# Performance work log

Hardware: AMD Instinct MI355X
Metric: run time of the kernel (lower is better)

## Reference

```python
import jax, jax.numpy as jnp
import numpy as np

B, N, C, H = 8, 4096, 384, 8
HD = C // H  # 48
KERNEL_EPS = 1e-3
EPS = 1e-8


def setup_inputs() -> dict:
    key = jax.random.key(0)
    k1, k2, k3, k4 = jax.random.split(key, 4)
    x = jax.random.normal(k1, (B, N, C), dtype=jnp.float32)
    Wqkv = jax.random.normal(k2, (3 * C, C), dtype=jnp.float32) * 0.02
    Wproj = jax.random.normal(k3, (C, C), dtype=jnp.float32) * 0.02
    bproj = jax.random.normal(k4, (C,), dtype=jnp.float32) * 0.02
    return {"x": x, "Wqkv": Wqkv, "Wproj": Wproj, "bproj": bproj}


def reference(x, Wqkv, Wproj, bproj):
    # qkv projection (no bias): (B,N,3C) -> (3,B,H,N,HD)
    qkv = jnp.einsum('bnc,dc->bnd', x, Wqkv).reshape(B, N, 3, H, HD)
    qkv = jnp.transpose(qkv, (2, 0, 3, 1, 4))
    q, k, v = qkv[0], qkv[1], qkv[2]

    # generalized_kernel with projection_matrix=None, kernel_fn=ReLU
    dn = HD ** (-0.25)  # data normalizer
    qp = jax.nn.relu(dn * q) + KERNEL_EPS  # (B,H,N,HD) feature map, m=HD
    kp = jax.nn.relu(dn * k) + KERNEL_EPS

    ks = kp.sum(axis=2)                              # (B,H,m)
    D = jnp.einsum('bhnm,bhm->bhn', qp, ks)          # (B,H,N)
    kptv = jnp.einsum('bhnd,bhnm->bhdm', v, kp)      # (B,H,HD,m)
    out = jnp.einsum('bhnm,bhdm->bhnd', qp, kptv) / (D[..., None] + EPS)

    # faithful to original: reshape (B,H,N,HD) -> (B,N,C) WITHOUT head transpose
    out = out.reshape(B, N, C)
    return jnp.einsum('bnc,dc->bnd', out, Wproj) + bproj
```

## Files before the change

kernel.cpp:

```cpp
#include <hip/hip_runtime.h>
#include <hip/hip_bf16.h>


typedef __attribute__((ext_vector_type(8))) short short8;
typedef __attribute__((ext_vector_type(4))) float floatx4;

#define MFMA(a, b, c) __builtin_amdgcn_mfma_f32_16x16x32_bf16((a), (b), (c), 0, 0, 0)

__device__ __forceinline__ unsigned short f2bf(float f) {
  union { float f; unsigned u; } x; x.f = f;
  unsigned r = x.u + 0x7FFFu + ((x.u >> 16) & 1u);
  return (unsigned short)(r >> 16);
}

__device__ __forceinline__ void cv4(const float* __restrict__ in, unsigned short* __restrict__ out, int i) {
  float4 v = *(const float4*)(in + i);
  uint2 o;
  o.x = (unsigned)f2bf(v.x) | ((unsigned)f2bf(v.y) << 16);
  o.y = (unsigned)f2bf(v.z) | ((unsigned)f2bf(v.w) << 16);
  *(uint2*)(out + i) = o;
}

__global__ void conv_w(const float* __restrict__ wq, const float* __restrict__ wp,
                       unsigned short* __restrict__ wqb, unsigned short* __restrict__ wpb,
                       float* __restrict__ accD) {
  const int tid = blockIdx.x * blockDim.x + threadIdx.x;
  const int stride = gridDim.x * blockDim.x * 4;
  for (int i = tid * 4; i < 442368; i += stride) cv4(wq, wqb, i);
  for (int i = tid * 4; i < 147456; i += stride) cv4(wp, wpb, i);
  float4 z = {0.f, 0.f, 0.f, 0.f};
  for (int i = tid * 4; i < 196608; i += stride) *(float4*)(accD + i) = z;
}

__global__ __launch_bounds__(256, 2) void gemm_qkv(
    const float* __restrict__ x,
    const unsigned short* __restrict__ Wq,
    unsigned short* __restrict__ qp,
    float* __restrict__ accD) {
  __shared__ unsigned short As[128 * 64];
  __shared__ unsigned short Bs[128 * 64];
  __shared__ unsigned short Tt[2][48 * 136];

  const int cpx = gridDim.x >> 3;
  const int bid = (blockIdx.x & 7) * cpx + (blockIdx.x >> 3);
  const int mt = bid / 11;
  const int j = bid - mt * 11;
  const int tid = threadIdx.x;
  const int w = tid >> 6, lane = tid & 63;
  const int wm = w >> 1, wn = w & 1;
  const int l15 = lane & 15, l4 = lane >> 4;
  const int isQ = (j < 3);
  const int h = j - 3;

  floatx4 zero = {0.f, 0.f, 0.f, 0.f};
  floatx4 acc[4][4];
#pragma unroll
  for (int i = 0; i < 4; ++i)
#pragma unroll
    for (int jj = 0; jj < 4; ++jj) acc[i][jj] = zero;

  const size_t Abase = (size_t)mt * 128 * 384;
  const int arow = tid >> 4;
  const int akf = (tid & 15) * 4;

  for (int k0 = 0; k0 < 384; k0 += 64) {
#pragma unroll
    for (int p = 0; p < 8; ++p) {
      int row = p * 16 + arow;
      float4 v = *(const float4*)&x[Abase + (size_t)row * 384 + k0 + akf];
      uint2 o;
      o.x = (unsigned)f2bf(v.x) | ((unsigned)f2bf(v.y) << 16);
      o.y = (unsigned)f2bf(v.z) | ((unsigned)f2bf(v.w) << 16);
      *(uint2*)&As[row * 64 + akf] = o;
    }
    if (isQ) {
      const size_t Bb = (size_t)(j * 128) * 384;
#pragma unroll
      for (int i = 0; i < 4; ++i) {
        int li = w * 256 + i * 64 + lane;
        int row = li >> 3, col = (li & 7) << 3;
        __builtin_amdgcn_global_load_lds(
            (const __attribute__((address_space(1))) void*)(Wq + Bb + (size_t)row * 384 + k0 + col),
            (__attribute__((address_space(3))) void*)&Bs[row * 64 + col], 16, 0, 0);
      }
    } else {
#pragma unroll
      for (int i = 0; i < 3; ++i) {
        int idx = i * 256 + tid;
        int row = idx >> 3, col = (idx & 7) << 3;
        int srow = (row < 48) ? (384 + h * 48 + row) : (720 + h * 48 + row);
        __builtin_amdgcn_global_load_lds(
            (const __attribute__((address_space(1))) void*)(Wq + (size_t)srow * 384 + k0 + col),
            (__attribute__((address_space(3))) void*)&Bs[row * 64 + col], 16, 0, 0);
      }
    }
    __syncthreads();
#pragma unroll
    for (int kk = 0; kk < 2; ++kk) {
      short8 a[4];
#pragma unroll
      for (int mf = 0; mf < 4; ++mf)
        a[mf] = *(const short8*)&As[(wm * 64 + mf * 16 + l15) * 64 + kk * 32 + l4 * 8];
      if (isQ) {
#pragma unroll
        for (int nf = 0; nf < 4; ++nf) {
          short8 b = *(const short8*)&Bs[(wn * 64 + nf * 16 + l15) * 64 + kk * 32 + l4 * 8];
#pragma unroll
          for (int mf = 0; mf < 4; ++mf) acc[mf][nf] = MFMA(a[mf], b, acc[mf][nf]);
        }
      } else {
#pragma unroll
        for (int nf = 0; nf < 3; ++nf) {
          short8 b = *(const short8*)&Bs[(wn * 48 + nf * 16 + l15) * 64 + kk * 32 + l4 * 8];
#pragma unroll
          for (int mf = 0; mf < 4; ++mf) acc[mf][nf] = MFMA(a[mf], b, acc[mf][nf]);
        }
      }
    }
    __syncthreads();
  }

  const float DN = 0.3799178430f;
  if (isQ) {
#pragma unroll
    for (int mf = 0; mf < 4; ++mf) {
#pragma unroll
      for (int nf = 0; nf < 4; ++nf) {
        int gm0 = mt * 128 + wm * 64 + mf * 16 + l4 * 4;
        int gn = j * 128 + wn * 64 + nf * 16 + l15;
#pragma unroll
        for (int r = 0; r < 4; ++r) {
          float v = fmaxf(acc[mf][nf][r] * DN, 0.f) + 1e-3f;
          qp[(size_t)(gm0 + r) * 384 + gn] = f2bf(v);
        }
      }
    }
  } else {
#pragma unroll
    for (int nf = 0; nf < 3; ++nf) {
#pragma unroll
      for (int mf = 0; mf < 4; ++mf) {
#pragma unroll
        for (int r = 0; r < 4; ++r) {
          float v = acc[mf][nf][r];
          if (wn == 0) v = fmaxf(v * DN, 0.f) + 1e-3f;
          Tt[wn][(nf * 16 + l15) * 136 + wm * 64 + mf * 16 + l4 * 4 + r] = f2bf(v);
        }
      }
    }
    __syncthreads();
    short8 ones;
    {
      unsigned short ov = (l15 == 0) ? (unsigned short)0x3F80 : (unsigned short)0;
#pragma unroll
      for (int e = 0; e < 8; ++e) ones[e] = (short)ov;
    }
    floatx4 acc2[3];
#pragma unroll
    for (int i = 0; i < 3; ++i) acc2[i] = zero;
#pragma unroll
    for (int c = 0; c < 4; ++c) {
      short8 af;
      if (w < 3)
        af = *(const short8*)&Tt[1][(w * 16 + l15) * 136 + c * 32 + l4 * 8];
      else
        af = ones;
#pragma unroll
      for (int mfr = 0; mfr < 3; ++mfr) {
        short8 bf8 = *(const short8*)&Tt[0][(mfr * 16 + l15) * 136 + c * 32 + l4 * 8];
        acc2[mfr] = MFMA(af, bf8, acc2[mfr]);
      }
    }
    float* dst = accD + (size_t)((mt >> 5) * 8 + h) * 3072;
    if (w < 3) {
#pragma unroll
      for (int mfr = 0; mfr < 3; ++mfr)
#pragma unroll
        for (int r = 0; r < 4; ++r)
          atomicAdd(&dst[(w * 16 + l4 * 4 + r) * 48 + mfr * 16 + l15], acc2[mfr][r]);
    } else if (l4 == 0) {
#pragma unroll
      for (int mfr = 0; mfr < 3; ++mfr)
        atomicAdd(&dst[48 * 48 + mfr * 16 + l15], acc2[mfr][0]);
    }
  }
}

__global__ __launch_bounds__(256, 2) void attn_out(
    const unsigned short* __restrict__ qp,
    const float* __restrict__ accD,
    unsigned short* __restrict__ outr) {
  const int bh = blockIdx.x >> 4, tg = blockIdx.x & 15;
  const int b = bh >> 3, h = bh & 7;
  const int tid = threadIdx.x, w = tid >> 6, lane = tid & 63;
  const int l15 = lane & 15, l4 = lane >> 4;
  const int t0 = tg * 256 + w * 64;

  short8 bfr[2][4];
#pragma unroll
  for (int kk = 0; kk < 2; ++kk) {
#pragma unroll
    for (int nf = 0; nf < 4; ++nf) {
      int row = nf * 16 + l15;
      int c0 = kk * 32 + l4 * 8;
      short8 f;
      if (kk == 1 && l4 >= 2) {
#pragma unroll
        for (int e = 0; e < 8; ++e) f[e] = 0;
      } else {
        const float* p = accD + (size_t)bh * 3072 + row * 48 + c0;
        float4 v0 = *(const float4*)p;
        float4 v1 = *(const float4*)(p + 4);
        f[0] = (short)f2bf(v0.x); f[1] = (short)f2bf(v0.y);
        f[2] = (short)f2bf(v0.z); f[3] = (short)f2bf(v0.w);
        f[4] = (short)f2bf(v1.x); f[5] = (short)f2bf(v1.y);
        f[6] = (short)f2bf(v1.z); f[7] = (short)f2bf(v1.w);
      }
      bfr[kk][nf] = f;
    }
  }

  floatx4 zero = {0.f, 0.f, 0.f, 0.f};
  floatx4 acc[4][4];
#pragma unroll
  for (int i = 0; i < 4; ++i)
#pragma unroll
    for (int j = 0; j < 4; ++j) acc[i][j] = zero;

  const size_t rb = (size_t)b * 4096;
#pragma unroll
  for (int mf = 0; mf < 4; ++mf) {
#pragma unroll
    for (int kk = 0; kk < 2; ++kk) {
      int tt = t0 + mf * 16 + l15;
      short8 a = *(const short8*)&qp[(rb + tt) * 384 + h * 48 + kk * 32 + l4 * 8];
#pragma unroll
      for (int nf = 0; nf < 4; ++nf)
        acc[mf][nf] = MFMA(a, bfr[kk][nf], acc[mf][nf]);
    }
  }

#pragma unroll
  for (int mf = 0; mf < 4; ++mf) {
    float den[4];
#pragma unroll
    for (int r = 0; r < 4; ++r)
      den[r] = __shfl(acc[mf][3][r], lane & 48, 64) + 1e-8f;
#pragma unroll
    for (int nf = 0; nf < 3; ++nf) {
#pragma unroll
      for (int r = 0; r < 4; ++r) {
        int tt = t0 + mf * 16 + l4 * 4 + r;
        int d = nf * 16 + l15;
        float v = acc[mf][nf][r] / den[r];
        int np = h * 512 + (tt >> 3);
        int cp = (tt & 7) * 48 + d;
        outr[(rb + np) * 384 + cp] = f2bf(v);
      }
    }
  }
}

__global__ __launch_bounds__(256, 2) void gemm_proj(
    const unsigned short* __restrict__ A,
    const unsigned short* __restrict__ Bt,
    float* __restrict__ Cout,
    const float* __restrict__ bias) {
  __shared__ unsigned short As[128 * 64];
  __shared__ unsigned short Bs[128 * 64];
  const int NT = 3;
  const int cpx = gridDim.x >> 3;
  const int bid = (blockIdx.x & 7) * cpx + (blockIdx.x >> 3);
  const int bn = bid % NT;
  const int bm = bid / NT;
  const int tid = threadIdx.x;
  const int w = tid >> 6, lane = tid & 63;
  const int wm = w >> 1, wn = w & 1;
  const int l15 = lane & 15, l4 = lane >> 4;

  floatx4 zero = {0.f, 0.f, 0.f, 0.f};
  floatx4 acc[4][4];
#pragma unroll
  for (int i = 0; i < 4; ++i)
#pragma unroll
    for (int j = 0; j < 4; ++j) acc[i][j] = zero;

  const int li0 = (w * 4) * 64 + lane;
  const size_t Abase = (size_t)(bm * 128) * 384;
  const size_t Bbase = (size_t)(bn * 128) * 384;

  for (int k0 = 0; k0 < 384; k0 += 64) {
#pragma unroll
    for (int i = 0; i < 4; ++i) {
      int li = li0 + i * 64;
      int row = li >> 3;
      int col = (li & 7) << 3;
      __builtin_amdgcn_global_load_lds(
          (const __attribute__((address_space(1))) void*)(A + Abase + (size_t)row * 384 + k0 + col),
          (__attribute__((address_space(3))) void*)&As[(w * 4 + i) * 512], 16, 0, 0);
      __builtin_amdgcn_global_load_lds(
          (const __attribute__((address_space(1))) void*)(Bt + Bbase + (size_t)row * 384 + k0 + col),
          (__attribute__((address_space(3))) void*)&Bs[(w * 4 + i) * 512], 16, 0, 0);
    }
    __syncthreads();
#pragma unroll
    for (int kk = 0; kk < 2; ++kk) {
      short8 a[4], b[4];
#pragma unroll
      for (int mf = 0; mf < 4; ++mf)
        a[mf] = *(const short8*)&As[(wm * 64 + mf * 16 + l15) * 64 + kk * 32 + l4 * 8];
#pragma unroll
      for (int nf = 0; nf < 4; ++nf)
        b[nf] = *(const short8*)&Bs[(wn * 64 + nf * 16 + l15) * 64 + kk * 32 + l4 * 8];
#pragma unroll
      for (int mf = 0; mf < 4; ++mf)
#pragma unroll
        for (int nf = 0; nf < 4; ++nf)
          acc[mf][nf] = MFMA(a[mf], b[nf], acc[mf][nf]);
    }
    __syncthreads();
  }

#pragma unroll
  for (int mf = 0; mf < 4; ++mf) {
#pragma unroll
    for (int nf = 0; nf < 4; ++nf) {
      int gm0 = bm * 128 + wm * 64 + mf * 16 + l4 * 4;
      int gn = bn * 128 + wn * 64 + nf * 16 + l15;
#pragma unroll
      for (int r = 0; r < 4; ++r)
        Cout[(size_t)(gm0 + r) * 384 + gn] = acc[mf][nf][r] + bias[gn];
    }
  }
}

extern "C" void kernel_launch(void* const* d_in, const int* in_sizes, int n_in,
                              void* d_out, int out_size, void* d_ws, size_t ws_size,
                              hipStream_t stream) {
  const float* x = (const float*)d_in[0];
  const float* Wqkv = (const float*)d_in[1];
  const float* Wproj = (const float*)d_in[2];
  const float* bproj = (const float*)d_in[3];

  char* ws = (char*)d_ws;
  unsigned short* qp = (unsigned short*)(ws);
  float* accD = (float*)(ws + 25165824);
  unsigned short* outr = (unsigned short*)(ws + 25952256);
  unsigned short* wqkvb = (unsigned short*)(ws + 51118080);
  unsigned short* wprojb = (unsigned short*)(ws + 52002816);

  conv_w<<<256, 256, 0, stream>>>(Wqkv, Wproj, wqkvb, wprojb, accD);
  gemm_qkv<<<2816, 256, 0, stream>>>(x, wqkvb, qp, accD);
  attn_out<<<1024, 256, 0, stream>>>(qp, accD, outr);
  gemm_proj<<<768, 256, 0, stream>>>(outr, wprojb, (float*)d_out, bproj);
}
```

Measured before the change: 207.4 us.

## Prefetch x tiles into registers, stage qp in LDS, use reciprocal for normalization

In the QKV GEMM, the next k-step's fp32 x tile is loaded into registers right after the barrier, so the global load overlaps the MFMA work. The bf16 conversion and LDS store of that tile move to the next iteration. The K/V feature-map stores to LDS are packed into 64-bit writes. In attn_out, each block's 256x48 qp tile is staged through padded shared memory instead of per-lane strided global loads, and the division by the denominator becomes a hardware reciprocal plus multiply, which slightly lowers precision and raises register use.

```diff
diff --git a/kernel.cpp b/kernel.cpp
--- a/kernel.cpp
+++ b/kernel.cpp
@@ -63,16 +63,12 @@
   const int arow = tid >> 4;
   const int akf = (tid & 15) * 4;
 
+  float4 xv[8];
+#pragma unroll
+  for (int p = 0; p < 8; ++p)
+    xv[p] = *(const float4*)&x[Abase + (size_t)(p * 16 + arow) * 384 + akf];
+
   for (int k0 = 0; k0 < 384; k0 += 64) {
-#pragma unroll
-    for (int p = 0; p < 8; ++p) {
-      int row = p * 16 + arow;
-      float4 v = *(const float4*)&x[Abase + (size_t)row * 384 + k0 + akf];
-      uint2 o;
-      o.x = (unsigned)f2bf(v.x) | ((unsigned)f2bf(v.y) << 16);
-      o.y = (unsigned)f2bf(v.z) | ((unsigned)f2bf(v.w) << 16);
-      *(uint2*)&As[row * 64 + akf] = o;
-    }
     if (isQ) {
       const size_t Bb = (size_t)(j * 128) * 384;
 #pragma unroll
@@ -94,7 +90,20 @@
             (__attribute__((address_space(3))) void*)&Bs[row * 64 + col], 16, 0, 0);
       }
     }
-    __syncthreads();
+#pragma unroll
+    for (int p = 0; p < 8; ++p) {
+      int row = p * 16 + arow;
+      uint2 o;
+      o.x = (unsigned)f2bf(xv[p].x) | ((unsigned)f2bf(xv[p].y) << 16);
+      o.y = (unsigned)f2bf(xv[p].z) | ((unsigned)f2bf(xv[p].w) << 16);
+      *(uint2*)&As[row * 64 + akf] = o;
+    }
+    __syncthreads();
+    if (k0 < 320) {
+#pragma unroll
+      for (int p = 0; p < 8; ++p)
+        xv[p] = *(const float4*)&x[Abase + (size_t)(p * 16 + arow) * 384 + k0 + 64 + akf];
+    }
 #pragma unroll
     for (int kk = 0; kk < 2; ++kk) {
       short8 a[4];
@@ -140,12 +149,18 @@
     for (int nf = 0; nf < 3; ++nf) {
 #pragma unroll
       for (int mf = 0; mf < 4; ++mf) {
-#pragma unroll
-        for (int r = 0; r < 4; ++r) {
-          float v = acc[mf][nf][r];
-          if (wn == 0) v = fmaxf(v * DN, 0.f) + 1e-3f;
-          Tt[wn][(nf * 16 + l15) * 136 + wm * 64 + mf * 16 + l4 * 4 + r] = f2bf(v);
+        float v0 = acc[mf][nf][0], v1 = acc[mf][nf][1];
+        float v2 = acc[mf][nf][2], v3 = acc[mf][nf][3];
+        if (wn == 0) {
+          v0 = fmaxf(v0 * DN, 0.f) + 1e-3f;
+          v1 = fmaxf(v1 * DN, 0.f) + 1e-3f;
+          v2 = fmaxf(v2 * DN, 0.f) + 1e-3f;
+          v3 = fmaxf(v3 * DN, 0.f) + 1e-3f;
         }
+        uint2 o;
+        o.x = (unsigned)f2bf(v0) | ((unsigned)f2bf(v1) << 16);
+        o.y = (unsigned)f2bf(v2) | ((unsigned)f2bf(v3) << 16);
+        *(uint2*)&Tt[wn][(nf * 16 + l15) * 136 + wm * 64 + mf * 16 + l4 * 4] = o;
       }
     }
     __syncthreads();
@@ -190,11 +205,13 @@
     const unsigned short* __restrict__ qp,
     const float* __restrict__ accD,
     unsigned short* __restrict__ outr) {
+  __shared__ unsigned short Qs[256 * 52 + 64];
   const int bh = blockIdx.x >> 4, tg = blockIdx.x & 15;
   const int b = bh >> 3, h = bh & 7;
   const int tid = threadIdx.x, w = tid >> 6, lane = tid & 63;
   const int l15 = lane & 15, l4 = lane >> 4;
   const int t0 = tg * 256 + w * 64;
+  const size_t rb = (size_t)b * 4096;
 
   short8 bfr[2][4];
 #pragma unroll
@@ -220,6 +237,18 @@
     }
   }
 
+#pragma unroll
+  for (int c = 0; c < 6; ++c) {
+    int idx = c * 256 + tid;
+    int row = idx / 6;
+    int part = idx - row * 6;
+    short8 v = *(const short8*)&qp[(rb + tg * 256 + row) * 384 + h * 48 + part * 8];
+    *(short8*)&Qs[row * 52 + part * 8] = v;
+  }
+  *(uint2*)&Qs[tid * 52 + 48] = (uint2){0u, 0u};
+  if (tid < 64) Qs[256 * 52 + tid] = 0;
+  __syncthreads();
+
   floatx4 zero = {0.f, 0.f, 0.f, 0.f};
   floatx4 acc[4][4];
 #pragma unroll
@@ -227,13 +256,11 @@
 #pragma unroll
     for (int j = 0; j < 4; ++j) acc[i][j] = zero;
 
-  const size_t rb = (size_t)b * 4096;
 #pragma unroll
   for (int mf = 0; mf < 4; ++mf) {
 #pragma unroll
     for (int kk = 0; kk < 2; ++kk) {
-      int tt = t0 + mf * 16 + l15;
-      short8 a = *(const short8*)&qp[(rb + tt) * 384 + h * 48 + kk * 32 + l4 * 8];
+      short8 a = *(const short8*)&Qs[(w * 64 + mf * 16 + l15) * 52 + kk * 32 + l4 * 8];
 #pragma unroll
       for (int nf = 0; nf < 4; ++nf)
         acc[mf][nf] = MFMA(a, bfr[kk][nf], acc[mf][nf]);
@@ -242,17 +269,19 @@
 
 #pragma unroll
   for (int mf = 0; mf < 4; ++mf) {
-    float den[4];
-#pragma unroll
-    for (int r = 0; r < 4; ++r)
-      den[r] = __shfl(acc[mf][3][r], lane & 48, 64) + 1e-8f;
+    float inv[4];
+#pragma unroll
+    for (int r = 0; r < 4; ++r) {
+      float den = __shfl(acc[mf][3][r], lane & 48, 64) + 1e-8f;
+      inv[r] = __builtin_amdgcn_rcpf(den);
+    }
 #pragma unroll
     for (int nf = 0; nf < 3; ++nf) {
 #pragma unroll
       for (int r = 0; r < 4; ++r) {
         int tt = t0 + mf * 16 + l4 * 4 + r;
         int d = nf * 16 + l15;
-        float v = acc[mf][nf][r] / den[r];
+        float v = acc[mf][nf][r] * inv[r];
         int np = h * 512 + (tt >> 3);
         int cp = (tt & 7) * 48 + d;
         outr[(rb + np) * 384 + cp] = f2bf(v);
```

New measurement: 195.8 us. 5.6% less time.
